# Kernel tuning notes

Hardware: AMD Instinct MI355X
Metric: run time of the kernel (lower is better)

Reference implementation:

```python
import jax, jax.numpy as jnp
import numpy as np

SEQ, BATCH, IN_DIM, HID, OUT_DIM = 2048, 128, 128, 256, 64


def setup_inputs() -> dict:
    key = jax.random.key(0)
    ks = jax.random.split(key, 7)
    s = 1.0 / np.sqrt(HID)
    x = jax.random.normal(ks[0], (SEQ, BATCH, IN_DIM), dtype=jnp.float32)
    W_ih = jax.random.uniform(ks[1], (4 * HID, IN_DIM), minval=-s, maxval=s, dtype=jnp.float32)
    W_hh = jax.random.uniform(ks[2], (4 * HID, HID), minval=-s, maxval=s, dtype=jnp.float32)
    b_ih = jax.random.uniform(ks[3], (4 * HID,), minval=-s, maxval=s, dtype=jnp.float32)
    b_hh = jax.random.uniform(ks[4], (4 * HID,), minval=-s, maxval=s, dtype=jnp.float32)
    W_out = jax.random.uniform(ks[5], (OUT_DIM, HID), minval=-s, maxval=s, dtype=jnp.float32)
    b_out = jax.random.uniform(ks[6], (OUT_DIM,), minval=-s, maxval=s, dtype=jnp.float32)
    return {"x": x, "W_ih": W_ih, "W_hh": W_hh, "b_ih": b_ih, "b_hh": b_hh,
            "W_out": W_out, "b_out": b_out}


def _lstm(x, W_ih, W_hh, b_ih, b_hh):
    # Precompute input contribution for all timesteps: [T, B, 4H]
    xg = jnp.einsum('tbi,gi->tbg', x, W_ih) + b_ih + b_hh
    H = W_hh.shape[1]
    B = x.shape[1]
    h0 = jnp.zeros((B, H), dtype=x.dtype)
    c0 = jnp.zeros((B, H), dtype=x.dtype)

    def step(carry, xg_t):
        h, c = carry
        gates = xg_t + h @ W_hh.T  # [B, 4H]
        i, f, g, o = jnp.split(gates, 4, axis=-1)  # PyTorch gate order i,f,g,o
        i = jax.nn.sigmoid(i)
        f = jax.nn.sigmoid(f)
        g = jnp.tanh(g)
        o = jax.nn.sigmoid(o)
        c_new = f * c + i * g
        h_new = o * jnp.tanh(c_new)
        return (h_new, c_new), h_new

    _, r_out = jax.lax.scan(step, (h0, c0), xg)  # r_out: [T, B, H]
    return r_out


def reference(x, W_ih, W_hh, b_ih, b_hh, W_out, b_out):
    r_out = _lstm(x, W_ih, W_hh, b_ih, b_hh)
    out = jnp.einsum('tbh,oh->tbo', r_out, W_out) + b_out  # [T, B, OUT]
    return out
```

## Files before the change

kernel.cpp:

```cpp
#include <hip/hip_runtime.h>
#include <stdint.h>


#define T_SEQ 2048
#define BATCH 128
#define IN_D  128
#define HID   256
#define OUTD  64

typedef _Float16 half2_t __attribute__((ext_vector_type(2)));

__device__ __forceinline__ float dot2f(uint32_t w, uint32_t h, float acc) {
#if __has_builtin(__builtin_amdgcn_fdot2)
  return __builtin_amdgcn_fdot2(__builtin_bit_cast(half2_t, w),
                                __builtin_bit_cast(half2_t, h), acc, false);
#else
  half2_t a = __builtin_bit_cast(half2_t, w);
  half2_t b = __builtin_bit_cast(half2_t, h);
  return acc + (float)a[0] * (float)b[0] + (float)a[1] * (float)b[1];
#endif
}

__device__ __forceinline__ uint32_t pack2(float a, float b) {
  union { _Float16 h[2]; uint32_t u; } u_;
  u_.h[0] = (_Float16)a; u_.h[1] = (_Float16)b;
  return u_.u;
}

__device__ __forceinline__ uint64_t ld64_ag(const uint64_t* p) {
  return __hip_atomic_load(p, __ATOMIC_RELAXED, __HIP_MEMORY_SCOPE_AGENT);
}
__device__ __forceinline__ void st64_ag(uint64_t* p, uint64_t v) {
  __hip_atomic_store(p, v, __ATOMIC_RELAXED, __HIP_MEMORY_SCOPE_AGENT);
}

__device__ __forceinline__ uint4 loadW8(const float* __restrict__ pw) {
  const float4 a = *(const float4*)pw;
  const float4 b = *(const float4*)(pw + 4);
  uint4 r;
  r.x = pack2(a.x, a.y); r.y = pack2(a.z, a.w);
  r.z = pack2(b.x, b.y); r.w = pack2(b.z, b.w);
  return r;
}

__device__ __forceinline__ float sigm(float v) { return 1.f / (1.f + __expf(-v)); }
__device__ __forceinline__ float tanhx(float v) {
  float a = fabsf(v);
  float e = __expf(2.f * a);
  float r = 1.f - 2.f / (e + 1.f);
  return v < 0.f ? -r : r;
}

#define D4(Wv, Hv, A)                       \
  A = dot2f(Wv.x, Hv.x, A);                 \
  A = dot2f(Wv.y, Hv.y, A);                 \
  A = dot2f(Wv.z, Hv.z, A);                 \
  A = dot2f(Wv.w, Hv.w, A);

#define PIN4(v) asm volatile("" : "+v"(v.x), "+v"(v.y), "+v"(v.z), "+v"(v.w));

#define XG_ALL(slotbase)                                                     \
  {                                                                          \
    const uint4* xp0 = (const uint4*)(xring + (slotbase)) + ks * 2;          \
    const uint4* xp1 = (const uint4*)(xring + (slotbase) + 64) + ks * 2;     \
    const uint4 xa = xp0[0], xb = xp0[1];                                    \
    const uint4 xc = xp1[0], xd = xp1[1];                                    \
    axg00 = 0.f; axg10 = 0.f; axg20 = 0.f; axg30 = 0.f;                      \
    axg01 = 0.f; axg11 = 0.f; axg21 = 0.f; axg31 = 0.f;                      \
    D4(X0_0, xa, axg00) D4(X0_1, xb, axg00)                                  \
    D4(X1_0, xa, axg10) D4(X1_1, xb, axg10)                                  \
    D4(X2_0, xa, axg20) D4(X2_1, xb, axg20)                                  \
    D4(X3_0, xa, axg30) D4(X3_1, xb, axg30)                                  \
    D4(X0_0, xc, axg01) D4(X0_1, xd, axg01)                                  \
    D4(X1_0, xc, axg11) D4(X1_1, xd, axg11)                                  \
    D4(X2_0, xc, axg21) D4(X2_1, xd, axg21)                                  \
    D4(X3_0, xc, axg31) D4(X3_1, xd, axg31)                                  \
  }

__global__ __launch_bounds__(512, 2)
void lstm_persist(const float* __restrict__ x,   const float* __restrict__ Wih,
                  const float* __restrict__ Whh, const float* __restrict__ bih,
                  const float* __restrict__ bhh, const float* __restrict__ Wout,
                  const float* __restrict__ bout_g, float* __restrict__ out,
                  uint64_t* exch)
{
  __shared__ alignas(16) uint32_t hbuf[2 * 128];
  __shared__ alignas(16) uint32_t xring[2 * 2 * 64];

  const int tid = threadIdx.x;
  const int w   = blockIdx.x;
  const int p   = w & 63;
  const int q   = w >> 6;
  const int jj  = tid >> 3;
  const int ks  = tid & 7;
  const int rbase = (q << 6) + jj;

  uint4 H0_0, H0_1, H0_2, H0_3, X0_0, X0_1;
  uint4 H1_0, H1_1, H1_2, H1_3, X1_0, X1_1;
  uint4 H2_0, H2_1, H2_2, H2_3, X2_0, X2_1;
  uint4 H3_0, H3_1, H3_2, H3_3, X3_0, X3_1;
#define LOADG(g)                                                 \
  { const int row = (g) * HID + rbase;                           \
    const float* ph = Whh + (size_t)row * HID + (ks << 5);       \
    H##g##_0 = loadW8(ph);      H##g##_1 = loadW8(ph + 8);       \
    H##g##_2 = loadW8(ph + 16); H##g##_3 = loadW8(ph + 24);      \
    const float* px = Wih + (size_t)row * IN_D + (ks << 4);      \
    X##g##_0 = loadW8(px);      X##g##_1 = loadW8(px + 8); }
  LOADG(0) LOADG(1) LOADG(2) LOADG(3)
#undef LOADG
  PIN4(H0_0) PIN4(H0_1) PIN4(H0_2) PIN4(H0_3) PIN4(X0_0) PIN4(X0_1)
  PIN4(H1_0) PIN4(H1_1) PIN4(H1_2) PIN4(H1_3) PIN4(X1_0) PIN4(X1_1)
  PIN4(H2_0) PIN4(H2_1) PIN4(H2_2) PIN4(H2_3) PIN4(X2_0) PIN4(X2_1)
  PIN4(H3_0) PIN4(H3_1) PIN4(H3_2) PIN4(H3_3) PIN4(X3_0) PIN4(X3_1)

  float b0 = bih[0 * HID + rbase] + bhh[0 * HID + rbase];
  float b1 = bih[1 * HID + rbase] + bhh[1 * HID + rbase];
  float b2 = bih[2 * HID + rbase] + bhh[2 * HID + rbase];
  float b3 = bih[3 * HID + rbase] + bhh[3 * HID + rbase];

  const int oo = tid >> 5, orow = (tid >> 4) & 1, os = tid & 15;
  uint4 woA, woB;
  {
    const float* wo = Wout + (size_t)((q << 4) + oo) * HID + (os << 4);
    const float4 v0 = *(const float4*)(wo + 0), v1 = *(const float4*)(wo + 4);
    const float4 v2 = *(const float4*)(wo + 8), v3 = *(const float4*)(wo + 12);
    woA.x = pack2(v0.x, v0.y); woA.y = pack2(v0.z, v0.w);
    woA.z = pack2(v1.x, v1.y); woA.w = pack2(v1.z, v1.w);
    woB.x = pack2(v2.x, v2.y); woB.y = pack2(v2.z, v2.w);
    woB.z = pack2(v3.x, v3.y); woB.w = pack2(v3.z, v3.w);
  }
  PIN4(woA) PIN4(woB)
  const float bo = bout_g[(q << 4) + oo];

  if (tid < 256) hbuf[tid] = 0u;
  if (tid < 128) {
    const int row = tid >> 6, cc = tid & 63;
    const float2 xv = *(const float2*)(x + (size_t)(2 * p + row) * IN_D + 2 * cc);
    xring[row * 64 + cc] = pack2(xv.x, xv.y);
  } else if (tid < 256) {
    const int i = tid - 128, row = i >> 6, cc = i & 63;
    const float2 xv = *(const float2*)(x + (size_t)BATCH * IN_D +
                                       (size_t)(2 * p + row) * IN_D + 2 * cc);
    xring[128 + row * 64 + cc] = pack2(xv.x, xv.y);
  }
  float c = 0.f;
  __syncthreads();

  const int pi  = tid - 64;
  const int pqq = pi >> 6, pl = pi & 63;
  const int pqp = pqq + (pqq >= q);
  const int pws = (pqp << 6) | p;

  float axg00, axg10, axg20, axg30, axg01, axg11, axg21, axg31;
  XG_ALL(0)

  for (int t = 0; t <= T_SEQ; ++t) {
    uint32_t xn = 0;
    uint32_t packed = 0;
    if (t < T_SEQ) {
      if (tid >= 256 && tid < 384 && (t + 2) < T_SEQ) {
        const int row = (tid - 256) >> 6, cc = (tid - 256) & 63;
        const float2 xv = *(const float2*)(x + (size_t)(t + 2) * BATCH * IN_D +
                                           (size_t)(2 * p + row) * IN_D + 2 * cc);
        xn = pack2(xv.x, xv.y);
      }
      float a00 = axg00, a10 = axg10, a20 = axg20, a30 = axg30;
      float a01 = axg01, a11 = axg11, a21 = axg21, a31 = axg31;
      {
        const uint4* hb = (const uint4*)hbuf + (ks << 2);
        const uint4 h0 = hb[0], h1 = hb[1], h2 = hb[2], h3 = hb[3];
        D4(H0_0, h0, a00) D4(H0_1, h1, a00) D4(H0_2, h2, a00) D4(H0_3, h3, a00)
        D4(H1_0, h0, a10) D4(H1_1, h1, a10) D4(H1_2, h2, a10) D4(H1_3, h3, a10)
        D4(H2_0, h0, a20) D4(H2_1, h1, a20) D4(H2_2, h2, a20) D4(H2_3, h3, a20)
        D4(H3_0, h0, a30) D4(H3_1, h1, a30) D4(H3_2, h2, a30) D4(H3_3, h3, a30)
      }
      {
        const uint4* hb = (const uint4*)hbuf + 32 + (ks << 2);
        const uint4 h0 = hb[0], h1 = hb[1], h2 = hb[2], h3 = hb[3];
        D4(H0_0, h0, a01) D4(H0_1, h1, a01) D4(H0_2, h2, a01) D4(H0_3, h3, a01)
        D4(H1_0, h0, a11) D4(H1_1, h1, a11) D4(H1_2, h2, a11) D4(H1_3, h3, a11)
        D4(H2_0, h0, a21) D4(H2_1, h1, a21) D4(H2_2, h2, a21) D4(H2_3, h3, a21)
        D4(H3_0, h0, a31) D4(H3_1, h1, a31) D4(H3_2, h2, a31) D4(H3_3, h3, a31)
      }
      float u0, u1, u2, u3;
      {
        const int r = ks & 1;
        float t0, t1;
        t0 = a00 + __shfl_xor(a00, 1, 64); t1 = a01 + __shfl_xor(a01, 1, 64);
        u0 = r ? t1 : t0;
        t0 = a10 + __shfl_xor(a10, 1, 64); t1 = a11 + __shfl_xor(a11, 1, 64);
        u1 = r ? t1 : t0;
        t0 = a20 + __shfl_xor(a20, 1, 64); t1 = a21 + __shfl_xor(a21, 1, 64);
        u2 = r ? t1 : t0;
        t0 = a30 + __shfl_xor(a30, 1, 64); t1 = a31 + __shfl_xor(a31, 1, 64);
        u3 = r ? t1 : t0;
      }
      u0 += __shfl_xor(u0, 2, 64); u0 += __shfl_xor(u0, 4, 64);
      u1 += __shfl_xor(u1, 2, 64); u1 += __shfl_xor(u1, 4, 64);
      u2 += __shfl_xor(u2, 2, 64); u2 += __shfl_xor(u2, 4, 64);
      u3 += __shfl_xor(u3, 2, 64); u3 += __shfl_xor(u3, 4, 64);
      if (ks < 2) {
        const int r = ks;
        const float iv = sigm(b0 + u0), fv = sigm(b1 + u1);
        const float gv = tanhx(b2 + u2), ov = sigm(b3 + u3);
        c = fv * c + iv * gv;
        const float hn = ov * tanhx(c);
        union { _Float16 h; unsigned short u; } cv; cv.h = (_Float16)hn;
        const uint32_t mine  = cv.u;
        const uint32_t other = (uint32_t)(unsigned short)__shfl_xor((int)mine, 8, 64);
        if (!(jj & 1)) {
          packed = mine | (other << 16);
          const uint64_t entry = ((uint64_t)(uint32_t)(t + 1) << 32) | packed;
          st64_ag(exch + (((size_t)w << 7) | ((t & 1) << 6)) + (r << 5) + (jj >> 1),
                  entry);
        }
      }
    }
    if (t >= 1) {
      const uint4* hq = (const uint4*)hbuf + orow * 32 + os * 2;
      const uint4 h0 = hq[0], h1 = hq[1];
      float oa = 0.f;
      oa = dot2f(woA.x, h0.x, oa); oa = dot2f(woA.y, h0.y, oa);
      oa = dot2f(woA.z, h0.z, oa); oa = dot2f(woA.w, h0.w, oa);
      oa = dot2f(woB.x, h1.x, oa); oa = dot2f(woB.y, h1.y, oa);
      oa = dot2f(woB.z, h1.z, oa); oa = dot2f(woB.w, h1.w, oa);
      oa += __shfl_xor(oa, 1, 64); oa += __shfl_xor(oa, 2, 64);
      oa += __shfl_xor(oa, 4, 64); oa += __shfl_xor(oa, 8, 64);
      if (os == 0)
        out[((size_t)(t - 1) * BATCH + 2 * p + orow) * OUTD + (q << 4) + oo] = oa + bo;
    }
    __syncthreads();
    if (t < T_SEQ) {
      if (ks < 2 && !(jj & 1))
        hbuf[ks * 128 + (q << 5) + (jj >> 1)] = packed;
      if (tid >= 256 && tid < 384 && (t + 2) < T_SEQ)
        xring[((t & 1) << 7) + (((tid - 256) >> 6) << 6) + ((tid - 256) & 63)] = xn;
      if (t + 1 < T_SEQ)
        XG_ALL(((t + 1) & 1) << 7)
      if (tid >= 64 && tid < 256) {
        const uint64_t* src = exch + (((size_t)pws << 7) | ((t & 1) << 6)) + pl;
        const uint32_t want = (uint32_t)(t + 1);
        uint64_t e;
        do { e = ld64_ag(src); } while ((uint32_t)(e >> 32) != want);
        hbuf[(pl >> 5) * 128 + (pqp << 5) + (pl & 31)] = (uint32_t)e;
      }
    }
    __syncthreads();
  }
}

extern "C" void kernel_launch(void* const* d_in, const int* in_sizes, int n_in,
                              void* d_out, int out_size, void* d_ws, size_t ws_size,
                              hipStream_t stream) {
  (void)in_sizes; (void)n_in; (void)out_size; (void)ws_size;
  const float* x    = (const float*)d_in[0];
  const float* Wih  = (const float*)d_in[1];
  const float* Whh  = (const float*)d_in[2];
  const float* bih  = (const float*)d_in[3];
  const float* bhh  = (const float*)d_in[4];
  const float* Wout = (const float*)d_in[5];
  const float* bout = (const float*)d_in[6];
  float* out = (float*)d_out;

  uint64_t* exch = (uint64_t*)d_ws;

  hipLaunchKernelGGL(lstm_persist, dim3(256), dim3(512), 0, stream,
                     x, Wih, Whh, bih, bhh, Wout, bout, out, exch);
}
```

Measured before the change: 4.912 ms.

## Map exchange groups onto same XCC and use non-coherent volatile exchange

Each block reads its XCC id at startup and claims a (p,q) role through atomic counters, so the four blocks that exchange hidden state tend to sit on the same XCC. A runtime handshake checks whether plain volatile loads and stores are visible among the group; if so, the per-step exchange uses volatile accesses instead of agent-scope atomics, aiming to cut cross-die coherence latency on the recurrence critical path. The hbuf layout is also permuted to reduce LDS bank conflicts. This adds a startup barrier, a memset, and reliance on cache behaviour that the handshake only tests empirically, so correctness depends on that test being reliable.

```diff
diff --git a/kernel.cpp b/kernel.cpp
--- a/kernel.cpp
+++ b/kernel.cpp
@@ -33,6 +33,16 @@
 __device__ __forceinline__ void st64_ag(uint64_t* p, uint64_t v) {
   __hip_atomic_store(p, v, __ATOMIC_RELAXED, __HIP_MEMORY_SCOPE_AGENT);
 }
+__device__ __forceinline__ uint32_t ld32_ag(const uint32_t* p) {
+  return __hip_atomic_load(p, __ATOMIC_RELAXED, __HIP_MEMORY_SCOPE_AGENT);
+}
+
+__device__ __forceinline__ uint64_t ld64_vol(const uint64_t* p) {
+  return *(const volatile uint64_t*)p;
+}
+__device__ __forceinline__ void st64_vol(uint64_t* p, uint64_t v) {
+  *(volatile uint64_t*)p = v;
+}
 
 __device__ __forceinline__ uint4 loadW8(const float* __restrict__ pw) {
   const float4 a = *(const float4*)pw;
@@ -49,6 +59,10 @@
   float e = __expf(2.f * a);
   float r = 1.f - 2.f / (e + 1.f);
   return v < 0.f ? -r : r;
+}
+
+__device__ __forceinline__ int hphys(int dl) {
+  return ((dl >> 2) & 3) * 32 + ((dl >> 4) << 2) + (dl & 3);
 }
 
 #define D4(Wv, Hv, A)                       \
@@ -77,23 +91,84 @@
     D4(X3_0, xc, axg31) D4(X3_1, xd, axg31)                                  \
   }
 
+#define MAGB 0x600DD00Dull
+#define MAGC 0xC0015EEDull
+#define XCC_GETREG_IMM 63508
+
 __global__ __launch_bounds__(512, 2)
 void lstm_persist(const float* __restrict__ x,   const float* __restrict__ Wih,
                   const float* __restrict__ Whh, const float* __restrict__ bih,
                   const float* __restrict__ bhh, const float* __restrict__ Wout,
                   const float* __restrict__ bout_g, float* __restrict__ out,
-                  uint64_t* exch)
+                  uint64_t* exch, uint64_t* hdr)
 {
   __shared__ alignas(16) uint32_t hbuf[2 * 128];
   __shared__ alignas(16) uint32_t xring[2 * 2 * 64];
+  __shared__ int sh_p, sh_q, sh_fast;
 
   const int tid = threadIdx.x;
   const int w   = blockIdx.x;
-  const int p   = w & 63;
-  const int q   = w >> 6;
+
+  if (tid == 0) {
+    int p, q, fast = 0;
+    if (hdr) {
+      uint32_t* h32  = (uint32_t*)hdr;
+      uint64_t* test = hdr + 8;
+      uint64_t* cons = hdr + 8 + 256;
+      uint32_t xcc = __builtin_amdgcn_s_getreg(XCC_GETREG_IMM) & 7u;
+      const int s = (int)atomicAdd(&h32[xcc], 1u);
+      __threadfence();
+      atomicAdd(&h32[8], 1u);
+      while (ld32_ag(&h32[8]) < 256u) { }
+      uint32_t c[8]; uint32_t tq = 0;
+      for (int i = 0; i < 8; ++i) { c[i] = ld32_ag(&h32[i]); tq += c[i] >> 2; }
+      if ((uint32_t)(s >> 2) < (c[xcc] >> 2)) {
+        uint32_t before = 0;
+        for (uint32_t i = 0; i < xcc; ++i) before += c[i] >> 2;
+        p = (int)(before + (uint32_t)(s >> 2)); q = s & 3;
+      } else {
+        uint32_t li = atomicAdd(&h32[9], 1u);
+        p = (int)(tq + (li >> 2)); q = (int)(li & 3);
+      }
+      int ok = 1;
+      st64_vol(&test[p * 4 + q], (MAGB << 32) | 1ull);
+      for (int m = 0; m < 4 && ok; ++m) {
+        if (m == q) continue;
+        int spins = 0; uint64_t e;
+        do {
+          e = ld64_vol(&test[p * 4 + m]);
+          if (++spins > 32768) { ok = 0; break; }
+        } while ((e >> 32) != MAGB);
+      }
+      st64_vol(&test[p * 4 + q], (MAGB << 32) | 2ull);
+      for (int m = 0; m < 4 && ok; ++m) {
+        if (m == q) continue;
+        int spins = 0; uint64_t e;
+        do {
+          e = ld64_vol(&test[p * 4 + m]);
+          if (++spins > 32768) { ok = 0; break; }
+        } while (e != ((MAGB << 32) | 2ull));
+      }
+      st64_ag(&cons[p * 4 + q], (MAGC << 32) | (uint64_t)(ok & 1));
+      fast = ok;
+      for (int m = 0; m < 4; ++m) {
+        if (m == q) continue;
+        uint64_t e;
+        do { e = ld64_ag(&cons[p * 4 + m]); } while ((e >> 32) != MAGC);
+        fast &= (int)(e & 1);
+      }
+    } else {
+      p = w & 63; q = w >> 6; fast = 0;
+    }
+    sh_p = p; sh_q = q; sh_fast = fast;
+  }
+  __syncthreads();
+  const int p = sh_p, q = sh_q, fastf = sh_fast;
+
   const int jj  = tid >> 3;
   const int ks  = tid & 7;
   const int rbase = (q << 6) + jj;
+  const int role  = (q << 6) | p;
 
   uint4 H0_0, H0_1, H0_2, H0_3, X0_0, X0_1;
   uint4 H1_0, H1_1, H1_2, H1_3, X1_0, X1_1;
@@ -131,6 +206,8 @@
   }
   PIN4(woA) PIN4(woB)
   const float bo = bout_g[(q << 4) + oo];
+  const int oadr0 = orow * 128 + (((os * 2)     & 3) << 5) + ((os >> 1) << 2);
+  const int oadr1 = orow * 128 + (((os * 2 + 1) & 3) << 5) + ((os >> 1) << 2);
 
   if (tid < 256) hbuf[tid] = 0u;
   if (tid < 128) {
@@ -149,7 +226,8 @@
   const int pi  = tid - 64;
   const int pqq = pi >> 6, pl = pi & 63;
   const int pqp = pqq + (pqq >= q);
-  const int pws = (pqp << 6) | p;
+  const int prole = (pqp << 6) | p;
+  const int dep_adr = (pl >> 5) * 128 + hphys((pqp << 5) + (pl & 31));
 
   float axg00, axg10, axg20, axg30, axg01, axg11, axg21, axg31;
   XG_ALL(0)
@@ -167,16 +245,22 @@
       float a00 = axg00, a10 = axg10, a20 = axg20, a30 = axg30;
       float a01 = axg01, a11 = axg11, a21 = axg21, a31 = axg31;
       {
-        const uint4* hb = (const uint4*)hbuf + (ks << 2);
-        const uint4 h0 = hb[0], h1 = hb[1], h2 = hb[2], h3 = hb[3];
+        const uint32_t* hb = hbuf;
+        const uint4 h0 = *(const uint4*)(hb +       (ks << 2));
+        const uint4 h1 = *(const uint4*)(hb +  32 + (ks << 2));
+        const uint4 h2 = *(const uint4*)(hb +  64 + (ks << 2));
+        const uint4 h3 = *(const uint4*)(hb +  96 + (ks << 2));
         D4(H0_0, h0, a00) D4(H0_1, h1, a00) D4(H0_2, h2, a00) D4(H0_3, h3, a00)
         D4(H1_0, h0, a10) D4(H1_1, h1, a10) D4(H1_2, h2, a10) D4(H1_3, h3, a10)
         D4(H2_0, h0, a20) D4(H2_1, h1, a20) D4(H2_2, h2, a20) D4(H2_3, h3, a20)
         D4(H3_0, h0, a30) D4(H3_1, h1, a30) D4(H3_2, h2, a30) D4(H3_3, h3, a30)
       }
       {
-        const uint4* hb = (const uint4*)hbuf + 32 + (ks << 2);
-        const uint4 h0 = hb[0], h1 = hb[1], h2 = hb[2], h3 = hb[3];
+        const uint32_t* hb = hbuf + 128;
+        const uint4 h0 = *(const uint4*)(hb +       (ks << 2));
+        const uint4 h1 = *(const uint4*)(hb +  32 + (ks << 2));
+        const uint4 h2 = *(const uint4*)(hb +  64 + (ks << 2));
+        const uint4 h3 = *(const uint4*)(hb +  96 + (ks << 2));
         D4(H0_0, h0, a01) D4(H0_1, h1, a01) D4(H0_2, h2, a01) D4(H0_3, h3, a01)
         D4(H1_0, h0, a11) D4(H1_1, h1, a11) D4(H1_2, h2, a11) D4(H1_3, h3, a11)
         D4(H2_0, h0, a21) D4(H2_1, h1, a21) D4(H2_2, h2, a21) D4(H2_3, h3, a21)
@@ -211,14 +295,15 @@
         if (!(jj & 1)) {
           packed = mine | (other << 16);
           const uint64_t entry = ((uint64_t)(uint32_t)(t + 1) << 32) | packed;
-          st64_ag(exch + (((size_t)w << 7) | ((t & 1) << 6)) + (r << 5) + (jj >> 1),
-                  entry);
+          uint64_t* dst =
+              exch + (((size_t)role << 7) | ((t & 1) << 6)) + (r << 5) + (jj >> 1);
+          if (fastf) st64_vol(dst, entry); else st64_ag(dst, entry);
         }
       }
     }
     if (t >= 1) {
-      const uint4* hq = (const uint4*)hbuf + orow * 32 + os * 2;
-      const uint4 h0 = hq[0], h1 = hq[1];
+      const uint4 h0 = *(const uint4*)(hbuf + oadr0);
+      const uint4 h1 = *(const uint4*)(hbuf + oadr1);
       float oa = 0.f;
       oa = dot2f(woA.x, h0.x, oa); oa = dot2f(woA.y, h0.y, oa);
       oa = dot2f(woA.z, h0.z, oa); oa = dot2f(woA.w, h0.w, oa);
@@ -232,17 +317,22 @@
     __syncthreads();
     if (t < T_SEQ) {
       if (ks < 2 && !(jj & 1))
-        hbuf[ks * 128 + (q << 5) + (jj >> 1)] = packed;
+        hbuf[ks * 128 + hphys((q << 5) + (jj >> 1))] = packed;
       if (tid >= 256 && tid < 384 && (t + 2) < T_SEQ)
         xring[((t & 1) << 7) + (((tid - 256) >> 6) << 6) + ((tid - 256) & 63)] = xn;
       if (t + 1 < T_SEQ)
         XG_ALL(((t + 1) & 1) << 7)
       if (tid >= 64 && tid < 256) {
-        const uint64_t* src = exch + (((size_t)pws << 7) | ((t & 1) << 6)) + pl;
+        const uint64_t* src =
+            exch + (((size_t)prole << 7) | ((t & 1) << 6)) + pl;
         const uint32_t want = (uint32_t)(t + 1);
         uint64_t e;
-        do { e = ld64_ag(src); } while ((uint32_t)(e >> 32) != want);
-        hbuf[(pl >> 5) * 128 + (pqp << 5) + (pl & 31)] = (uint32_t)e;
+        if (fastf) {
+          do { e = ld64_vol(src); } while ((uint32_t)(e >> 32) != want);
+        } else {
+          do { e = ld64_ag(src);  } while ((uint32_t)(e >> 32) != want);
+        }
+        hbuf[dep_adr] = (uint32_t)e;
       }
     }
     __syncthreads();
@@ -252,7 +342,7 @@
 extern "C" void kernel_launch(void* const* d_in, const int* in_sizes, int n_in,
                               void* d_out, int out_size, void* d_ws, size_t ws_size,
                               hipStream_t stream) {
-  (void)in_sizes; (void)n_in; (void)out_size; (void)ws_size;
+  (void)in_sizes; (void)n_in; (void)out_size;
   const float* x    = (const float*)d_in[0];
   const float* Wih  = (const float*)d_in[1];
   const float* Whh  = (const float*)d_in[2];
@@ -262,8 +352,15 @@
   const float* bout = (const float*)d_in[6];
   float* out = (float*)d_out;
 
+  const size_t RING_BYTES = 256u * 1024u;
+  const size_t HDR_BYTES  = 8u * 1024u;
   uint64_t* exch = (uint64_t*)d_ws;
+  uint64_t* hdr  = nullptr;
+  if (ws_size >= RING_BYTES + HDR_BYTES) {
+    hdr = exch + (RING_BYTES / 8);
+    hipMemsetAsync((void*)hdr, 0, HDR_BYTES, stream);
+  }
 
   hipLaunchKernelGGL(lstm_persist, dim3(256), dim3(512), 0, stream,
-                     x, Wih, Whh, bih, bhh, Wout, bout, out, exch);
-}
+                     x, Wih, Whh, bih, bhh, Wout, bout, out, exch, hdr);
+}
```

New measurement: 5.368 ms. 1.09x slower.
